# Optimization experiments

Hardware: AMD Instinct MI355X
Metric: run time of the kernel (lower is better)

The kernel has to match this reference:

```python
import jax, jax.numpy as jnp
import numpy as np

N_NODES = 100000
N_INCID = 2000000
HIDDEN = 128
N_HE = 100000


def setup_inputs() -> dict:
    key = jax.random.key(0)
    k1, k2, k3 = jax.random.split(key, 3)
    node_feats = jax.random.normal(k1, (N_NODES, HIDDEN), dtype=jnp.float32)
    hyperedge_index = jax.random.randint(k2, (2, N_INCID), 0, N_HE, dtype=jnp.int64)
    # xavier_uniform for Linear(hidden,1): bound = sqrt(6/(hidden+1))
    bound = float(np.sqrt(6.0 / (HIDDEN + 1)))
    W = jax.random.uniform(k3, (1, HIDDEN), dtype=jnp.float32, minval=-bound, maxval=bound)
    return {"node_feats": node_feats, "hyperedge_index": hyperedge_index,
            "num_hyperedges": N_HE, "W": W}


def reference(node_feats, hyperedge_index, num_hyperedges, W):
    node_idx = hyperedge_index[0]
    he_idx = hyperedge_index[1]
    gathered = node_feats[node_idx]                      # [E, D]
    scores = jnp.einsum('ed,d->e', gathered, W[0])       # [E]
    # segment softmax over hyperedges
    seg_max = jax.ops.segment_max(scores, he_idx, num_segments=num_hyperedges)
    seg_max = jnp.where(jnp.isfinite(seg_max), seg_max, 0.0)  # empty segments
    w = jnp.exp(scores - seg_max[he_idx])                # [E]
    denom = jax.ops.segment_sum(w, he_idx, num_segments=num_hyperedges)
    w_norm = w / jnp.maximum(denom, 1e-20)[he_idx]       # [E]
    # weighted scatter-sum; empty hyperedges stay zero
    out = jax.ops.segment_sum(w_norm[:, None] * gathered, he_idx,
                              num_segments=num_hyperedges)  # [H, D]
    return out
```

## Files before the change

### kernel.cpp

```cpp
#include <hip/hip_runtime.h>
#include <hip/hip_fp16.h>
#include <math.h>

#define N_NODES 100000
#define N_INCID 2000000
#define HIDDEN  128
#define N_HE    100000

#define CHAINS 4
#define EPB 1024
#define FILL_BLOCKS ((N_INCID + EPB - 1) / EPB)
#define PREP_BLOCKS ((N_NODES + 3) / 4)

typedef float vf4 __attribute__((ext_vector_type(4)));

__device__ inline float4 h4_to_f4(unsigned a_, unsigned b_) {
    __half2 a = *(__half2*)&a_;
    __half2 b = *(__half2*)&b_;
    float2 fa = __half22float2(a);
    float2 fb = __half22float2(b);
    return make_float4(fa.x, fa.y, fb.x, fb.y);
}

__global__ void prep_fill_kernel(const float* __restrict__ nf,
                                 const float* __restrict__ W,
                                 const int* __restrict__ idx,
                                 float* __restrict__ en,
                                 __half2* __restrict__ nfh2,
                                 int* __restrict__ head,
                                 int2* __restrict__ next8) {
    int b = blockIdx.x;
    if (b < FILL_BLOCKS) {
        int base = b * EPB;
        int e = base + threadIdx.x;
        if (base + EPB <= N_INCID) {
            int he[4], nd[4], prev[4];
            #pragma unroll
            for (int k = 0; k < 4; ++k) {
                he[k] = idx[N_INCID + e + 256 * k];
                nd[k] = idx[e + 256 * k];
            }
            #pragma unroll
            for (int k = 0; k < 4; ++k) {
                int ek = e + 256 * k;
                prev[k] = atomicExch(&head[(he[k] << 2) | (ek & 3)], ek);
            }
            #pragma unroll
            for (int k = 0; k < 4; ++k)
                next8[e + 256 * k] = make_int2(nd[k], prev[k]);
        } else {
            #pragma unroll
            for (int k = 0; k < 4; ++k) {
                int ek = e + 256 * k;
                if (ek < N_INCID) {
                    int he = idx[N_INCID + ek];
                    int nd = idx[ek];
                    int prev = atomicExch(&head[(he << 2) | (ek & 3)], ek);
                    next8[ek] = make_int2(nd, prev);
                }
            }
        }
    } else {
        int wave = threadIdx.x >> 6, lane = threadIdx.x & 63;
        int n = (b - FILL_BLOCKS) * 4 + wave;
        if (n >= N_NODES) return;
        const float2* nf2 = (const float2*)nf;
        const float2* w2  = (const float2*)W;
        float2 v = nf2[(size_t)n * 64 + lane];
        float2 w = w2[lane];
        float p = v.x * w.x + v.y * w.y;
        #pragma unroll
        for (int o = 32; o > 0; o >>= 1) p += __shfl_xor(p, o, 64);
        if (lane == 0) en[n] = __expf(p);
        nfh2[(size_t)n * 64 + lane] = __floats2half2_rn(v.x, v.y);
    }
}

__global__ void compute_kernel_w(const int* __restrict__ head,
                                 const int2* __restrict__ next8,
                                 const float* __restrict__ en,
                                 const uint4* __restrict__ nfq,
                                 float* __restrict__ out) {
    int wave = threadIdx.x >> 6, lane = threadIdx.x & 63;
    int he = blockIdx.x * 4 + wave;
    int q16 = lane >> 4, l16 = lane & 15;

    const long long* __restrict__ nxt = (const long long*)next8;

    int e = head[(he << 2) | q16];
    float4 acc0 = make_float4(0.f, 0.f, 0.f, 0.f);
    float4 acc1 = make_float4(0.f, 0.f, 0.f, 0.f);
    float den = 0.f;

    while (e >= 0) {
        long long q = nxt[e];
        int nd = (int)q;
        float w = en[nd];
        uint4 r = nfq[(size_t)nd * 16 + l16];
        float4 a = h4_to_f4(r.x, r.y);
        float4 bq = h4_to_f4(r.z, r.w);
        acc0.x += w * a.x;  acc0.y += w * a.y;
        acc0.z += w * a.z;  acc0.w += w * a.w;
        acc1.x += w * bq.x; acc1.y += w * bq.y;
        acc1.z += w * bq.z; acc1.w += w * bq.w;
        den += w;
        e = (int)(q >> 32);
    }

    #pragma unroll
    for (int o = 16; o <= 32; o <<= 1) {
        acc0.x += __shfl_xor(acc0.x, o, 64); acc0.y += __shfl_xor(acc0.y, o, 64);
        acc0.z += __shfl_xor(acc0.z, o, 64); acc0.w += __shfl_xor(acc0.w, o, 64);
        acc1.x += __shfl_xor(acc1.x, o, 64); acc1.y += __shfl_xor(acc1.y, o, 64);
        acc1.z += __shfl_xor(acc1.z, o, 64); acc1.w += __shfl_xor(acc1.w, o, 64);
        den += __shfl_xor(den, o, 64);
    }

    if (lane < 16) {
        float inv = 1.0f / fmaxf(den, 1e-20f);
        vf4 o0 = { acc0.x * inv, acc0.y * inv, acc0.z * inv, acc0.w * inv };
        vf4 o1 = { acc1.x * inv, acc1.y * inv, acc1.z * inv, acc1.w * inv };
        float* op = out + (size_t)he * 128 + l16 * 8;
        __builtin_nontemporal_store(o0, (vf4*)op);
        __builtin_nontemporal_store(o1, (vf4*)(op + 4));
    }
}

extern "C" void kernel_launch(void* const* d_in, const int* in_sizes, int n_in,
                              void* d_out, int out_size, void* d_ws, size_t ws_size,
                              hipStream_t stream) {
    const float* nf  = (const float*)d_in[0];
    const int*   idx = (const int*)d_in[1];
    const float* W   = (const float*)d_in[3];
    float* out = (float*)d_out;
    char* ws = (char*)d_ws;

    int*     head  = (int*)(ws + 0);
    float*   en    = (float*)(ws + 1600000);
    __half2* nfh2  = (__half2*)(ws + 2000000);
    int2*    next8 = (int2*)(ws + 27600000);

    hipMemsetAsync(head, 0xFF, CHAINS * N_HE * sizeof(int), stream);
    prep_fill_kernel<<<FILL_BLOCKS + PREP_BLOCKS, 256, 0, stream>>>(
        nf, W, idx, en, nfh2, head, next8);
    compute_kernel_w<<<(N_HE + 3) / 4, 256, 0, stream>>>(
        head, next8, en, (const uint4*)nfh2, out);
}
```

Before: 310.7 us.

## Fuse memset, fill/prep and compute into one cooperative persistent kernel

Replaces the memset plus two kernel launches with one cooperative kernel that uses grid-wide syncs between phases: head initialization, linked-list fill plus node prep, and per-hyperedge accumulation. Persistent blocks loop over work units with a grid sized from occupancy (256 CUs times blocks per CU, capped at 8). This is meant to remove launch gaps and memset overhead. In exchange it adds grid.sync costs and loses the overlap the separate launches had, and persistent grid-stride scheduling may balance the uneven hyperedge chains less well.

```diff
diff --git a/kernel.cpp b/kernel.cpp
--- a/kernel.cpp
+++ b/kernel.cpp
@@ -1,6 +1,9 @@
 #include <hip/hip_runtime.h>
 #include <hip/hip_fp16.h>
+#include <hip/hip_cooperative_groups.h>
 #include <math.h>
+
+namespace cg = cooperative_groups;
 
 #define N_NODES 100000
 #define N_INCID 2000000
@@ -9,8 +12,10 @@
 
 #define CHAINS 4
 #define EPB 1024
-#define FILL_BLOCKS ((N_INCID + EPB - 1) / EPB)
-#define PREP_BLOCKS ((N_NODES + 3) / 4)
+#define FILL_UNITS ((N_INCID + EPB - 1) / EPB)
+#define PREP_UNITS ((N_NODES + 3) / 4)
+#define COMP_UNITS ((N_HE + 3) / 4)
+#define HEAD_INTS (CHAINS * N_HE)
 
 typedef float vf4 __attribute__((ext_vector_type(4)));
 
@@ -22,15 +27,26 @@
     return make_float4(fa.x, fa.y, fb.x, fb.y);
 }
 
-__global__ void prep_fill_kernel(const float* __restrict__ nf,
-                                 const float* __restrict__ W,
-                                 const int* __restrict__ idx,
-                                 float* __restrict__ en,
-                                 __half2* __restrict__ nfh2,
-                                 int* __restrict__ head,
-                                 int2* __restrict__ next8) {
-    int b = blockIdx.x;
-    if (b < FILL_BLOCKS) {
+__global__ void mega_kernel(const float* __restrict__ nf,
+                            const float* __restrict__ W,
+                            const int* __restrict__ idx,
+                            float* __restrict__ en,
+                            __half2* __restrict__ nfh2,
+                            int* __restrict__ head,
+                            int2* __restrict__ next8,
+                            float* __restrict__ out) {
+    cg::grid_group grid = cg::this_grid();
+    const int nb = gridDim.x;
+    const int wave = threadIdx.x >> 6, lane = threadIdx.x & 63;
+
+    {
+        int4* h4p = (int4*)head;
+        for (int i = blockIdx.x * 256 + threadIdx.x; i < HEAD_INTS / 4; i += nb * 256)
+            h4p[i] = make_int4(-1, -1, -1, -1);
+    }
+    grid.sync();
+
+    for (int b = blockIdx.x; b < FILL_UNITS; b += nb) {
         int base = b * EPB;
         int e = base + threadIdx.x;
         if (base + EPB <= N_INCID) {
@@ -53,76 +69,79 @@
             for (int k = 0; k < 4; ++k) {
                 int ek = e + 256 * k;
                 if (ek < N_INCID) {
-                    int he = idx[N_INCID + ek];
+                    int heq = idx[N_INCID + ek];
                     int nd = idx[ek];
-                    int prev = atomicExch(&head[(he << 2) | (ek & 3)], ek);
+                    int prev = atomicExch(&head[(heq << 2) | (ek & 3)], ek);
                     next8[ek] = make_int2(nd, prev);
                 }
             }
         }
-    } else {
-        int wave = threadIdx.x >> 6, lane = threadIdx.x & 63;
-        int n = (b - FILL_BLOCKS) * 4 + wave;
-        if (n >= N_NODES) return;
+    }
+
+    {
         const float2* nf2 = (const float2*)nf;
         const float2* w2  = (const float2*)W;
-        float2 v = nf2[(size_t)n * 64 + lane];
         float2 w = w2[lane];
-        float p = v.x * w.x + v.y * w.y;
-        #pragma unroll
-        for (int o = 32; o > 0; o >>= 1) p += __shfl_xor(p, o, 64);
-        if (lane == 0) en[n] = __expf(p);
-        nfh2[(size_t)n * 64 + lane] = __floats2half2_rn(v.x, v.y);
+        for (int u = blockIdx.x; u < PREP_UNITS; u += nb) {
+            int n = u * 4 + wave;
+            if (n < N_NODES) {
+                float2 v = nf2[(size_t)n * 64 + lane];
+                float p = v.x * w.x + v.y * w.y;
+                #pragma unroll
+                for (int o = 32; o > 0; o >>= 1) p += __shfl_xor(p, o, 64);
+                if (lane == 0) en[n] = __expf(p);
+                nfh2[(size_t)n * 64 + lane] = __floats2half2_rn(v.x, v.y);
+            }
+        }
     }
-}
+    grid.sync();
 
-__global__ void compute_kernel_w(const int* __restrict__ head,
-                                 const int2* __restrict__ next8,
-                                 const float* __restrict__ en,
-                                 const uint4* __restrict__ nfq,
-                                 float* __restrict__ out) {
-    int wave = threadIdx.x >> 6, lane = threadIdx.x & 63;
-    int he = blockIdx.x * 4 + wave;
-    int q16 = lane >> 4, l16 = lane & 15;
+    {
+        const long long* __restrict__ nxt = (const long long*)next8;
+        const uint4* __restrict__ nfq = (const uint4*)nfh2;
+        int q16 = lane >> 4, l16 = lane & 15;
 
-    const long long* __restrict__ nxt = (const long long*)next8;
+        for (int u = blockIdx.x; u < COMP_UNITS; u += nb) {
+            int he = u * 4 + wave;
 
-    int e = head[(he << 2) | q16];
-    float4 acc0 = make_float4(0.f, 0.f, 0.f, 0.f);
-    float4 acc1 = make_float4(0.f, 0.f, 0.f, 0.f);
-    float den = 0.f;
+            int e = head[(he << 2) | q16];
+            float4 acc0 = make_float4(0.f, 0.f, 0.f, 0.f);
+            float4 acc1 = make_float4(0.f, 0.f, 0.f, 0.f);
+            float den = 0.f;
 
-    while (e >= 0) {
-        long long q = nxt[e];
-        int nd = (int)q;
-        float w = en[nd];
-        uint4 r = nfq[(size_t)nd * 16 + l16];
-        float4 a = h4_to_f4(r.x, r.y);
-        float4 bq = h4_to_f4(r.z, r.w);
-        acc0.x += w * a.x;  acc0.y += w * a.y;
-        acc0.z += w * a.z;  acc0.w += w * a.w;
-        acc1.x += w * bq.x; acc1.y += w * bq.y;
-        acc1.z += w * bq.z; acc1.w += w * bq.w;
-        den += w;
-        e = (int)(q >> 32);
-    }
+            while (e >= 0) {
+                long long q = nxt[e];
+                int nd = (int)q;
+                float w = en[nd];
+                uint4 r = nfq[(size_t)nd * 16 + l16];
+                float4 a = h4_to_f4(r.x, r.y);
+                float4 bq = h4_to_f4(r.z, r.w);
+                acc0.x += w * a.x;  acc0.y += w * a.y;
+                acc0.z += w * a.z;  acc0.w += w * a.w;
+                acc1.x += w * bq.x; acc1.y += w * bq.y;
+                acc1.z += w * bq.z; acc1.w += w * bq.w;
+                den += w;
+                e = (int)(q >> 32);
+            }
 
-    #pragma unroll
-    for (int o = 16; o <= 32; o <<= 1) {
-        acc0.x += __shfl_xor(acc0.x, o, 64); acc0.y += __shfl_xor(acc0.y, o, 64);
-        acc0.z += __shfl_xor(acc0.z, o, 64); acc0.w += __shfl_xor(acc0.w, o, 64);
-        acc1.x += __shfl_xor(acc1.x, o, 64); acc1.y += __shfl_xor(acc1.y, o, 64);
-        acc1.z += __shfl_xor(acc1.z, o, 64); acc1.w += __shfl_xor(acc1.w, o, 64);
-        den += __shfl_xor(den, o, 64);
-    }
+            #pragma unroll
+            for (int o = 16; o <= 32; o <<= 1) {
+                acc0.x += __shfl_xor(acc0.x, o, 64); acc0.y += __shfl_xor(acc0.y, o, 64);
+                acc0.z += __shfl_xor(acc0.z, o, 64); acc0.w += __shfl_xor(acc0.w, o, 64);
+                acc1.x += __shfl_xor(acc1.x, o, 64); acc1.y += __shfl_xor(acc1.y, o, 64);
+                acc1.z += __shfl_xor(acc1.z, o, 64); acc1.w += __shfl_xor(acc1.w, o, 64);
+                den += __shfl_xor(den, o, 64);
+            }
 
-    if (lane < 16) {
-        float inv = 1.0f / fmaxf(den, 1e-20f);
-        vf4 o0 = { acc0.x * inv, acc0.y * inv, acc0.z * inv, acc0.w * inv };
-        vf4 o1 = { acc1.x * inv, acc1.y * inv, acc1.z * inv, acc1.w * inv };
-        float* op = out + (size_t)he * 128 + l16 * 8;
-        __builtin_nontemporal_store(o0, (vf4*)op);
-        __builtin_nontemporal_store(o1, (vf4*)(op + 4));
+            if (lane < 16) {
+                float inv = 1.0f / fmaxf(den, 1e-20f);
+                vf4 o0 = { acc0.x * inv, acc0.y * inv, acc0.z * inv, acc0.w * inv };
+                vf4 o1 = { acc1.x * inv, acc1.y * inv, acc1.z * inv, acc1.w * inv };
+                float* op = out + (size_t)he * 128 + l16 * 8;
+                __builtin_nontemporal_store(o0, (vf4*)op);
+                __builtin_nontemporal_store(o1, (vf4*)(op + 4));
+            }
+        }
     }
 }
 
@@ -140,9 +159,18 @@
     __half2* nfh2  = (__half2*)(ws + 2000000);
     int2*    next8 = (int2*)(ws + 27600000);
 
-    hipMemsetAsync(head, 0xFF, CHAINS * N_HE * sizeof(int), stream);
-    prep_fill_kernel<<<FILL_BLOCKS + PREP_BLOCKS, 256, 0, stream>>>(
-        nf, W, idx, en, nfh2, head, next8);
-    compute_kernel_w<<<(N_HE + 3) / 4, 256, 0, stream>>>(
-        head, next8, en, (const uint4*)nfh2, out);
+    static int grid_blocks = 0;
+    if (grid_blocks == 0) {
+        int occ = 0;
+        (void)hipOccupancyMaxActiveBlocksPerMultiprocessor(&occ, mega_kernel, 256, 0);
+        if (occ < 1) occ = 1;
+        if (occ > 8) occ = 8;
+        grid_blocks = 256 * occ;
+    }
+
+    void* args[] = { (void*)&nf, (void*)&W, (void*)&idx, (void*)&en,
+                     (void*)&nfh2, (void*)&head, (void*)&next8, (void*)&out };
+    (void)hipLaunchCooperativeKernel((const void*)mega_kernel,
+                                     dim3(grid_blocks), dim3(256),
+                                     args, 0, stream);
 }
```

Measured after the change: 653.3 us. +110.3%, slower.
